# Optimization experiments

Hardware: AMD Instinct MI355X
Metric: run time of the kernel (lower is better)

The kernel has to match this reference:

```python
import jax, jax.numpy as jnp
import numpy as np

B, N, D, H, CD = 2, 2048, 1024, 16, 3
HD = D // H


def setup_inputs() -> dict:
    key = jax.random.key(0)
    ks = jax.random.split(key, 6)
    x = jax.random.normal(ks[0], (B, N, D), dtype=jnp.float32)
    coords = jax.random.normal(ks[1], (B, N, CD), dtype=jnp.float32)
    attn_bias = jax.random.normal(ks[2], (N, N), dtype=jnp.float32) * 0.1
    Wqkv = jax.random.normal(ks[3], (D, 3 * D), dtype=jnp.float32) * (1.0 / np.sqrt(D))
    bqkv = jnp.zeros((3 * D,), dtype=jnp.float32)
    rel_weight = jax.random.normal(ks[4], (H, CD), dtype=jnp.float32) * 0.02
    return {"x": x, "coords": coords, "attn_bias": attn_bias, "Wqkv": Wqkv,
            "bqkv": bqkv, "rel_weight": rel_weight}


def reference(x, coords, attn_bias, Wqkv, bqkv, rel_weight):
    b, n, d = x.shape
    h, hd = H, HD
    qkv = x @ Wqkv + bqkv                       # (B,N,3D)
    q, k, v = jnp.split(qkv, 3, axis=-1)
    # reshape_for_mha: (B,N,D) -> (B,H,N,hd)
    def heads(t):
        return t.reshape(b, n, h, hd).transpose(0, 2, 1, 3)
    qh, kh, vh = heads(q), heads(k), heads(v)
    # coord_proj[b,h,n] = coords[b,n,:] @ rel_weight[h,:]
    coord_proj = jnp.einsum('bnc,hc->bhn', coords.astype(jnp.float32), rel_weight)
    # flex_attention: scale by 1/sqrt(head_dim) BEFORE score_mod
    scores = jnp.einsum('bhqd,bhkd->bhqk', qh, kh) / np.sqrt(hd)
    scores = scores + coord_proj[:, :, :, None] - coord_proj[:, :, None, :]
    scores = scores + attn_bias[None, None, :, :]   # '2d' additive mask bias
    attn = jax.nn.softmax(scores, axis=-1)
    yh = jnp.einsum('bhqk,bhkd->bhqd', attn, vh)    # (B,H,N,hd)
    return yh.transpose(0, 2, 1, 3).reshape(b, n, d)
```

## Files before the change

kernel.cpp:

```cpp
#include <hip/hip_runtime.h>
#include <hip/hip_bf16.h>
#include <math.h>

typedef __hip_bfloat16 bf16;
typedef __bf16  bf16x8 __attribute__((ext_vector_type(8)));
typedef float   f32x4  __attribute__((ext_vector_type(4)));

#define BB 2
#define NN 2048
#define DD 1024
#define HH 16
#define HD 64
#define LOG2E   1.44269504f
#define SCALE_Q 0.18033688f

__device__ __forceinline__ void glds16(const bf16* g, bf16* l) {
    __builtin_amdgcn_global_load_lds((const __attribute__((address_space(1))) void*)g,
                                     (__attribute__((address_space(3))) void*)l, 16, 0, 0);
}
__device__ __forceinline__ unsigned short bfu(float x) {
    bf16 b = __float2bfloat16(x);
    return __builtin_bit_cast(unsigned short, b);
}

__global__ __launch_bounds__(256) void prep(const float* __restrict__ x,
                                            const float* __restrict__ bias,
                                            const float* __restrict__ W,
                                            const float* __restrict__ coords,
                                            const float* __restrict__ relw,
                                            bf16* __restrict__ xb,
                                            unsigned* __restrict__ pbh,
                                            bf16* __restrict__ Wt,
                                            bf16* __restrict__ cpn) {
    __shared__ bf16 tsm[64][65];
    const int bid = blockIdx.x, tid = threadIdx.x;
    if (bid < 2048) {
        size_t i = ((size_t)bid * 256 + tid) * 8;
        float4 a = *(const float4*)(x + i);
        float4 b = *(const float4*)(x + i + 4);
        bf16 t[8];
        t[0] = __float2bfloat16(a.x); t[1] = __float2bfloat16(a.y);
        t[2] = __float2bfloat16(a.z); t[3] = __float2bfloat16(a.w);
        t[4] = __float2bfloat16(b.x); t[5] = __float2bfloat16(b.y);
        t[6] = __float2bfloat16(b.z); t[7] = __float2bfloat16(b.w);
        *(int4*)(xb + i) = *(int4*)t;
    } else if (bid < 3072) {
        int tt   = (bid - 2048) * 256 + tid;
        int lane = tt & 63;
        int wave = (tt >> 6) & 7;
        int kt   = (tt >> 9) & 31;
        int Qb   = tt >> 14;
        int quad = lane >> 4, l15 = lane & 15;
        int q    = Qb * 128 + wave * 16 + l15;
        const float* brow = bias + (size_t)q * NN + kt * 64 + quad * 8;
        unsigned pk[8];
#pragma unroll
        for (int g = 0; g < 4; ++g) {
            int off = (g >> 1) * 32 + (g & 1) * 4;
            const float4 bv = *(const float4*)(brow + off);
            pk[g * 2]     = (unsigned)bfu(LOG2E * bv.x) | ((unsigned)bfu(LOG2E * bv.y) << 16);
            pk[g * 2 + 1] = (unsigned)bfu(LOG2E * bv.z) | ((unsigned)bfu(LOG2E * bv.w) << 16);
        }
        int4* dst = (int4*)(pbh + (size_t)tt * 8);
        dst[0] = ((int4*)pk)[0];
        dst[1] = ((int4*)pk)[1];
    } else if (bid < 3840) {
        int idx = bid - 3072;
        int n0 = (idx % 48) * 64;
        int k0 = (idx / 48) * 64;
        int tx = tid & 63, tg = tid >> 6;
#pragma unroll
        for (int i = 0; i < 16; ++i) {
            int r = tg + i * 4;
            tsm[r][tx] = __float2bfloat16(W[(size_t)(k0 + r) * 3072 + n0 + tx]);
        }
        __syncthreads();
#pragma unroll
        for (int i = 0; i < 16; ++i) {
            int r = tg + i * 4;
            Wt[(size_t)(n0 + r) * 1024 + k0 + tx] = tsm[tx][r];
        }
    } else {
        int idx = (bid - 3840) * 256 + tid;
        int n  = idx & (NN - 1);
        int bh = idx >> 11;
        int h  = bh & (HH - 1);
        int b  = bh >> 4;
        float acc = 0.f;
#pragma unroll
        for (int c = 0; c < 3; ++c)
            acc += coords[(size_t)(b * NN + n) * 3 + c] * relw[h * 3 + c];
        cpn[idx] = __float2bfloat16(-LOG2E * acc);
    }
}

__global__ __launch_bounds__(256) void qkv_gemm(const bf16* __restrict__ X,
                                                const bf16* __restrict__ W,
                                                const float* __restrict__ bq,
                                                bf16* __restrict__ qo,
                                                bf16* __restrict__ ko,
                                                bf16* __restrict__ vt) {
    __shared__ __align__(16) bf16 As[128 * 32];
    __shared__ __align__(16) bf16 Bs[128 * 32];
    const int tid  = threadIdx.x;
    const int gid  = blockIdx.x + blockIdx.y * 24;
    const int xcd  = gid & 7;
    const int idx  = gid >> 3;
    const int n0   = (idx >> 2) * 128;
    const int m0   = (xcd * 4 + (idx & 3)) * 128;
    const int wave = tid >> 6, lane = tid & 63, l15 = lane & 15, quad = lane >> 4;
    const int wm   = wave >> 1, wn = wave & 1;

    f32x4 acc[4][4];
    const f32x4 z4 = {0.f, 0.f, 0.f, 0.f};
#pragma unroll
    for (int i = 0; i < 4; ++i)
#pragma unroll
        for (int j = 0; j < 4; ++j) acc[i][j] = z4;

    for (int kt = 0; kt < 1024; kt += 32) {
        __syncthreads();
#pragma unroll
        for (int j = 0; j < 2; ++j) {
            int s   = (wave * 2 + j) * 64 + lane;
            int row = s >> 2;
            int c   = (s & 3) ^ ((row >> 1) & 3);
            glds16(X + (size_t)(m0 + row) * 1024 + kt + c * 8, As + (wave * 2 + j) * 512);
            glds16(W + (size_t)(n0 + row) * 1024 + kt + c * 8, Bs + (wave * 2 + j) * 512);
        }
        __syncthreads();

        bf16x8 a[4], b[4];
#pragma unroll
        for (int mt = 0; mt < 4; ++mt) {
            int ra = wm * 64 + mt * 16 + l15;
            a[mt] = *(const bf16x8*)&As[ra * 32 + ((quad ^ ((ra >> 1) & 3)) * 8)];
        }
#pragma unroll
        for (int nt = 0; nt < 4; ++nt) {
            int rb = wn * 64 + nt * 16 + l15;
            b[nt] = *(const bf16x8*)&Bs[rb * 32 + ((quad ^ ((rb >> 1) & 3)) * 8)];
        }
#pragma unroll
        for (int mt = 0; mt < 4; ++mt)
#pragma unroll
            for (int nt = 0; nt < 4; ++nt)
                acc[mt][nt] = __builtin_amdgcn_mfma_f32_16x16x32_bf16(a[mt], b[nt], acc[mt][nt], 0, 0, 0);
    }

#pragma unroll
    for (int nt = 0; nt < 4; ++nt) {
        int c    = n0 + wn * 64 + nt * 16 + l15;
        int tsel = c >> 10;
        int rem  = c & 1023;
        int h    = rem >> 6, d = rem & 63;
        float bias = bq[c];
        float qs   = (tsel == 0) ? SCALE_Q : 1.0f;
#pragma unroll
        for (int mt = 0; mt < 4; ++mt)
#pragma unroll
            for (int r = 0; r < 4; ++r) {
                int m = m0 + wm * 64 + mt * 16 + quad * 4 + r;
                int b = m >> 11, n = m & (NN - 1);
                bf16 val = __float2bfloat16((acc[mt][nt][r] + bias) * qs);
                if (tsel == 2)
                    vt[((size_t)(b * HH + h) * HD + d) * NN + n] = val;
                else
                    ((tsel == 1) ? ko : qo)[((size_t)(b * HH + h) * NN + n) * HD + d] = val;
            }
    }
}

__global__ __launch_bounds__(512, 4) void attn(const bf16* __restrict__ Q,
                                               const bf16* __restrict__ K,
                                               const bf16* __restrict__ Vt_g,
                                               const bf16* __restrict__ cpn_g,
                                               const unsigned* __restrict__ pbh,
                                               float* __restrict__ out) {
    __shared__ __align__(16) bf16 Ks[2][64 * 64];
    __shared__ __align__(16) bf16 Vs[2][64 * 64];
    __shared__ __align__(16) bf16 cpl[NN];
    const int tid  = threadIdx.x;
    const int Qb   = blockIdx.x;
    const int bh   = blockIdx.y;
    const int b    = bh >> 4, h = bh & 15;
    const int q0   = Qb * 128;
    const int wave = tid >> 6, lane = tid & 63, l15 = lane & 15, quad = lane >> 4;
    const size_t base = (size_t)bh * NN * HD;

    if (wave < 4)
        glds16(cpn_g + bh * NN + (wave * 64 + lane) * 8, cpl + wave * 512);

    const int qrow = q0 + wave * 16 + l15;
    bf16x8 qf0 = *(const bf16x8*)&Q[base + (size_t)qrow * HD + quad * 8];
    bf16x8 qf1 = *(const bf16x8*)&Q[base + (size_t)qrow * HD + 32 + quad * 8];

    const int ps    = wave * 64 + lane;
    const int prow  = ps >> 3;
    const int pcolV = (ps & 7) ^ (prow & 7);
    const int pcolK = (ps & 7) ^ ((prow & 3) | (((prow >> 3) & 1) << 2));

    glds16(K    + base + (size_t)prow * HD + pcolK * 8, Ks[0] + wave * 512);
    glds16(Vt_g + base + (size_t)prow * NN + pcolV * 8, Vs[0] + wave * 512);

    const unsigned* bptr = pbh + ((((size_t)Qb * 32) * 8 + wave) * 64 + lane) * 8;
    unsigned bvA[8], bvB[8];
    *(int4*)&bvA[0] = ((const int4*)bptr)[0];
    *(int4*)&bvA[4] = ((const int4*)bptr)[1];

    const int lrow = ((l15 >> 2) << 3) + (l15 & 3);
    const int fK   = (l15 & 3) | (((l15 >> 2) & 1) << 2);
    const int ck0  = (quad ^ fK) * 8;
    const int ck1  = ((4 + quad) ^ fK) * 8;

    const f32x4 z4 = {0.f, 0.f, 0.f, 0.f};
    float l_acc = 0.f;
    f32x4 o[4];
#pragma unroll
    for (int t = 0; t < 4; ++t) o[t] = z4;

#define ATTN_TILE(T, CUR, BVC, BVN)                                               \
    {                                                                             \
        __syncthreads();     \
        if ((T) < 31) {                   \
            int kk1 = ((T) + 1) * 64;                                             \
            glds16(K    + base + (size_t)(kk1 + prow) * HD + pcolK * 8,           \
                   Ks[(CUR) ^ 1] + wave * 512);                                   \
            glds16(Vt_g + base + (size_t)prow * NN + kk1 + pcolV * 8,             \
                   Vs[(CUR) ^ 1] + wave * 512);                                   \
            const unsigned* bp = bptr + (size_t)((T) + 1) * 4096;                 \
            *(int4*)&BVN[0] = ((const int4*)bp)[0];                               \
            *(int4*)&BVN[4] = ((const int4*)bp)[1];                               \
        }                                                                         \
          \
          \
        unsigned w32[8];                                                          \
        _Pragma("unroll")                                                         \
        for (int g = 0; g < 4; ++g) {                                             \
            const int kb = (g >> 1) * 32 + (g & 1) * 4;                           \
            ushort4 mgu = *(const ushort4*)&cpl[(T) * 64 + kb + quad * 8];        \
            unsigned ba = BVC[g * 2], bb2 = BVC[g * 2 + 1];                       \
            f32x4 c0;                                                             \
            c0[0] = __builtin_bit_cast(float, ba << 16)                           \
                  + __builtin_bit_cast(float, (unsigned)mgu.x << 16);             \
            c0[1] = __builtin_bit_cast(float, ba & 0xffff0000u)                   \
                  + __builtin_bit_cast(float, (unsigned)mgu.y << 16);             \
            c0[2] = __builtin_bit_cast(float, bb2 << 16)                          \
                  + __builtin_bit_cast(float, (unsigned)mgu.z << 16);             \
            c0[3] = __builtin_bit_cast(float, bb2 & 0xffff0000u)                  \
                  + __builtin_bit_cast(float, (unsigned)mgu.w << 16);             \
            int krow = kb + lrow;                                                 \
            bf16x8 k0 = *(const bf16x8*)&Ks[(CUR)][krow * 64 + ck0];              \
            bf16x8 k1 = *(const bf16x8*)&Ks[(CUR)][krow * 64 + ck1];              \
            f32x4 s4 = __builtin_amdgcn_mfma_f32_16x16x32_bf16(k0, qf0, c0, 0, 0, 0);      \
            s4 = __builtin_amdgcn_mfma_f32_16x16x32_bf16(k1, qf1, s4, 0, 0, 0);   \
            f32x4 e;                                                              \
            e[0] = __builtin_amdgcn_exp2f(s4[0]);                                 \
            e[1] = __builtin_amdgcn_exp2f(s4[1]);                                 \
            e[2] = __builtin_amdgcn_exp2f(s4[2]);                                 \
            e[3] = __builtin_amdgcn_exp2f(s4[3]);                                 \
            l_acc += (e[0] + e[1]) + (e[2] + e[3]);                               \
            w32[g * 2]     = (unsigned)bfu(e[0]) | ((unsigned)bfu(e[1]) << 16);   \
            w32[g * 2 + 1] = (unsigned)bfu(e[2]) | ((unsigned)bfu(e[3]) << 16);   \
        }                                                                         \
                  \
        union { unsigned u[4]; bf16x8 v; } B0, B1;                                \
        B0.u[0] = w32[0]; B0.u[1] = w32[1]; B0.u[2] = w32[2]; B0.u[3] = w32[3];   \
        B1.u[0] = w32[4]; B1.u[1] = w32[5]; B1.u[2] = w32[6]; B1.u[3] = w32[7];   \
                                         \
        __builtin_amdgcn_s_setprio(1);                                            \
        _Pragma("unroll")                                                         \
        for (int tt = 0; tt < 4; ++tt) {                                          \
            int drow = tt * 16 + l15, sw2 = drow & 7;                             \
            bf16x8 v0 = *(const bf16x8*)&Vs[(CUR)][drow * 64 + ((quad ^ sw2) * 8)];        \
            bf16x8 v1 = *(const bf16x8*)&Vs[(CUR)][drow * 64 + (((4 + quad) ^ sw2) * 8)];  \
            o[tt] = __builtin_amdgcn_mfma_f32_16x16x32_bf16(v0, B0.v, o[tt], 0, 0, 0);     \
            o[tt] = __builtin_amdgcn_mfma_f32_16x16x32_bf16(v1, B1.v, o[tt], 0, 0, 0);     \
        }                                                                         \
        __builtin_amdgcn_s_setprio(0);                                            \
    }

    for (int t = 0; t < 32; t += 2) {
        ATTN_TILE(t,     0, bvA, bvB)
        ATTN_TILE(t + 1, 1, bvB, bvA)
    }
#undef ATTN_TILE

    l_acc += __shfl_xor(l_acc, 16, 64);
    l_acc += __shfl_xor(l_acc, 32, 64);
    const float inv = 1.0f / l_acc;

    const int qq = q0 + wave * 16 + l15;
#pragma unroll
    for (int tt = 0; tt < 4; ++tt) {
        f32x4 ov;
        ov[0] = o[tt][0] * inv; ov[1] = o[tt][1] * inv;
        ov[2] = o[tt][2] * inv; ov[3] = o[tt][3] * inv;
        *(f32x4*)&out[((size_t)(b * NN + qq)) * DD + h * HD + tt * 16 + quad * 4] = ov;
    }
}

extern "C" void kernel_launch(void* const* d_in, const int* in_sizes, int n_in,
                              void* d_out, int out_size, void* d_ws, size_t ws_size,
                              hipStream_t stream) {
    const float* x      = (const float*)d_in[0];
    const float* coords = (const float*)d_in[1];
    const float* abias  = (const float*)d_in[2];
    const float* Wqkv   = (const float*)d_in[3];
    const float* bqkv   = (const float*)d_in[4];
    const float* relw   = (const float*)d_in[5];
    float* out = (float*)d_out;

    char* ws = (char*)d_ws;
    bf16*     xb  = (bf16*)(ws);
    bf16*     qw  = (bf16*)(ws + 8388608);
    bf16*     kw  = (bf16*)(ws + 16777216);
    bf16*     vt  = (bf16*)(ws + 25165824);
    bf16*     Wt  = (bf16*)(ws + 33554432);
    unsigned* pbh = (unsigned*)(ws + 39845888);
    bf16*     cpb = (bf16*)(ws + 56623104);

    prep    <<<dim3(4096),   256, 0, stream>>>(x, abias, Wqkv, coords, relw,
                                               xb, pbh, Wt, cpb);
    qkv_gemm<<<dim3(24, 32), 256, 0, stream>>>(xb, Wt, bqkv, qw, kw, vt);
    attn    <<<dim3(16, 32), 512, 0, stream>>>(qw, kw, vt, cpb, pbh, out);
}
```

Measured before the change: 191.9 us.

## Software-pipeline PV MFMA of previous tile with QK MFMA of current tile

Restructures the attention tile loop so the P·V matrix multiplies for tile T-1 are interleaved with the Q·K matrix multiplies for tile T, while exp2 and bf16 packing for tile T run afterwards. V fragments are loaded from LDS into registers at the end of each tile and consumed in the next, with a peeled first tile and an epilogue for the last PV. The aim is to hide the exp/softmax latency behind independent MFMA work. In exchange it needs more vector registers for the carried P and V fragments, which could lower occupancy.

```diff
diff --git a/kernel.cpp b/kernel.cpp
--- a/kernel.cpp
+++ b/kernel.cpp
@@ -219,7 +219,10 @@
 #pragma unroll
     for (int t = 0; t < 4; ++t) o[t] = z4;
 
-#define ATTN_TILE(T, CUR, BVC, BVN)                                               \
+    union { unsigned u[4]; bf16x8 v; } pB0, pB1;
+    bf16x8 pvf0[4], pvf1[4];
+
+#define ATTN_TILE(T, CUR, BVC, BVN, FIRST)                                        \
     {                                                                             \
         __syncthreads();     \
         if ((T) < 31) {                   \
@@ -232,9 +235,9 @@
             *(int4*)&BVN[0] = ((const int4*)bp)[0];                               \
             *(int4*)&BVN[4] = ((const int4*)bp)[1];                               \
         }                                                                         \
-          \
-          \
-        unsigned w32[8];                                                          \
+                 \
+        f32x4 s4v[4];                                                             \
+        __builtin_amdgcn_s_setprio(1);                                            \
         _Pragma("unroll")                                                         \
         for (int g = 0; g < 4; ++g) {                                             \
             const int kb = (g >> 1) * 32 + (g & 1) * 4;                           \
@@ -252,39 +255,50 @@
             int krow = kb + lrow;                                                 \
             bf16x8 k0 = *(const bf16x8*)&Ks[(CUR)][krow * 64 + ck0];              \
             bf16x8 k1 = *(const bf16x8*)&Ks[(CUR)][krow * 64 + ck1];              \
-            f32x4 s4 = __builtin_amdgcn_mfma_f32_16x16x32_bf16(k0, qf0, c0, 0, 0, 0);      \
-            s4 = __builtin_amdgcn_mfma_f32_16x16x32_bf16(k1, qf1, s4, 0, 0, 0);   \
+            s4v[g] = __builtin_amdgcn_mfma_f32_16x16x32_bf16(k0, qf0, c0, 0, 0, 0);        \
+            s4v[g] = __builtin_amdgcn_mfma_f32_16x16x32_bf16(k1, qf1, s4v[g], 0, 0, 0);    \
+            if (!(FIRST)) {                                                       \
+                o[g] = __builtin_amdgcn_mfma_f32_16x16x32_bf16(pvf0[g], pB0.v, o[g], 0, 0, 0); \
+                o[g] = __builtin_amdgcn_mfma_f32_16x16x32_bf16(pvf1[g], pB1.v, o[g], 0, 0, 0); \
+            }                                                                     \
+        }                                                                         \
+        __builtin_amdgcn_s_setprio(0);                                            \
+                         \
+        _Pragma("unroll")                                                         \
+        for (int g = 0; g < 4; ++g) {                                             \
             f32x4 e;                                                              \
-            e[0] = __builtin_amdgcn_exp2f(s4[0]);                                 \
-            e[1] = __builtin_amdgcn_exp2f(s4[1]);                                 \
-            e[2] = __builtin_amdgcn_exp2f(s4[2]);                                 \
-            e[3] = __builtin_amdgcn_exp2f(s4[3]);                                 \
+            e[0] = __builtin_amdgcn_exp2f(s4v[g][0]);                             \
+            e[1] = __builtin_amdgcn_exp2f(s4v[g][1]);                             \
+            e[2] = __builtin_amdgcn_exp2f(s4v[g][2]);                             \
+            e[3] = __builtin_amdgcn_exp2f(s4v[g][3]);                             \
             l_acc += (e[0] + e[1]) + (e[2] + e[3]);                               \
-            w32[g * 2]     = (unsigned)bfu(e[0]) | ((unsigned)bfu(e[1]) << 16);   \
-            w32[g * 2 + 1] = (unsigned)bfu(e[2]) | ((unsigned)bfu(e[3]) << 16);   \
+            unsigned w0 = (unsigned)bfu(e[0]) | ((unsigned)bfu(e[1]) << 16);      \
+            unsigned w1 = (unsigned)bfu(e[2]) | ((unsigned)bfu(e[3]) << 16);      \
+            if (g < 2) { pB0.u[g * 2] = w0; pB0.u[g * 2 + 1] = w1; }              \
+            else       { pB1.u[(g - 2) * 2] = w0; pB1.u[(g - 2) * 2 + 1] = w1; }  \
         }                                                                         \
-                  \
-        union { unsigned u[4]; bf16x8 v; } B0, B1;                                \
-        B0.u[0] = w32[0]; B0.u[1] = w32[1]; B0.u[2] = w32[2]; B0.u[3] = w32[3];   \
-        B1.u[0] = w32[4]; B1.u[1] = w32[5]; B1.u[2] = w32[6]; B1.u[3] = w32[7];   \
-                                         \
-        __builtin_amdgcn_s_setprio(1);                                            \
+                   \
         _Pragma("unroll")                                                         \
         for (int tt = 0; tt < 4; ++tt) {                                          \
             int drow = tt * 16 + l15, sw2 = drow & 7;                             \
-            bf16x8 v0 = *(const bf16x8*)&Vs[(CUR)][drow * 64 + ((quad ^ sw2) * 8)];        \
-            bf16x8 v1 = *(const bf16x8*)&Vs[(CUR)][drow * 64 + (((4 + quad) ^ sw2) * 8)];  \
-            o[tt] = __builtin_amdgcn_mfma_f32_16x16x32_bf16(v0, B0.v, o[tt], 0, 0, 0);     \
-            o[tt] = __builtin_amdgcn_mfma_f32_16x16x32_bf16(v1, B1.v, o[tt], 0, 0, 0);     \
+            pvf0[tt] = *(const bf16x8*)&Vs[(CUR)][drow * 64 + ((quad ^ sw2) * 8)];         \
+            pvf1[tt] = *(const bf16x8*)&Vs[(CUR)][drow * 64 + (((4 + quad) ^ sw2) * 8)];   \
         }                                                                         \
-        __builtin_amdgcn_s_setprio(0);                                            \
-    }
-
-    for (int t = 0; t < 32; t += 2) {
-        ATTN_TILE(t,     0, bvA, bvB)
-        ATTN_TILE(t + 1, 1, bvB, bvA)
+    }
+
+    ATTN_TILE(0, 0, bvA, bvB, 1)
+    ATTN_TILE(1, 1, bvB, bvA, 0)
+    for (int t = 2; t < 32; t += 2) {
+        ATTN_TILE(t,     0, bvA, bvB, 0)
+        ATTN_TILE(t + 1, 1, bvB, bvA, 0)
     }
 #undef ATTN_TILE
+
+#pragma unroll
+    for (int tt = 0; tt < 4; ++tt) {
+        o[tt] = __builtin_amdgcn_mfma_f32_16x16x32_bf16(pvf0[tt], pB0.v, o[tt], 0, 0, 0);
+        o[tt] = __builtin_amdgcn_mfma_f32_16x16x32_bf16(pvf1[tt], pB1.v, o[tt], 0, 0, 0);
+    }
 
     l_acc += __shfl_xor(l_acc, 16, 64);
     l_acc += __shfl_xor(l_acc, 32, 64);
```

Result: no change. 189.5 us (-1.3%).
